# Optimization experiments

Hardware: AMD Instinct MI355X
Metric: run time of the kernel (lower is better)

Reference implementation:

```python
import jax, jax.numpy as jnp
import numpy as np

LN2 = 0.6931471805599453

def ssp(x):
    # 'shifted_sp' activation: softplus(x) - log(2)
    return jax.nn.softplus(x) - LN2

def _res_chain(x, W1, b1, W2, b2):
    # PhysNetResidual chain: x <- lin2(ssp(lin1(ssp(x)))) + x
    # W1/W2: [n_res, F, F], b1/b2: [n_res, F]
    for j in range(W1.shape[0]):
        h = ssp(x) @ W1[j] + b1[j]
        x = ssp(h) @ W2[j] + b2[j] + x
    return x

def _physnet_module(feat, radial_aev, idx12, p):
    (W_I, b_I, W_J, b_J, W_gate, gvec, W_int, b_int,
     ri_W1, ri_b1, ri_W2, ri_b2,
     ra_W1, ra_b1, ra_W2, ra_b2,
     ro_W1, ro_b1, ro_W2, ro_b2, W_out, b_out) = p
    N, F = feat.shape
    # self term (no species are dummy -> non_dummy indexing is identity)
    h_self = ssp(ssp(feat) @ W_I + b_I)                       # [N,F]
    # pair messages
    gate = radial_aev @ W_gate                                 # [P,F] (no bias)
    f12 = feat[idx12]                                          # [2,P,F] gather
    fm = ssp(ssp(f12) @ W_J + b_J)                             # [2,P,F]
    pair_msg = gate[None] * fm                                 # [2,P,F]
    proto = jnp.zeros_like(feat).at[idx12.reshape(-1)].add(
        pair_msg.reshape(-1, F))                               # scatter-add
    proto = proto + h_self
    msg = _res_chain(proto, ri_W1, ri_b1, ri_W2, ri_b2)
    feat2 = feat * gvec + ssp(msg) @ W_int + b_int
    feat2 = _res_chain(feat2, ra_W1, ra_b1, ra_W2, ra_b2)
    e = ssp(_res_chain(feat2, ro_W1, ro_b1, ro_W2, ro_b2)) @ W_out + b_out  # [N]
    return e, feat2

def setup_inputs() -> dict:
    key = jax.random.key(0)
    L, F, R = 5, 128, 64
    M, A = 128, 64
    N = M * A
    P = 400000
    ks = jax.random.split(key, 20)
    s = 0.05  # small weight scale keeps activations stable across 5 modules
    inp = {
        'species': jax.random.randint(ks[0], (M, A), 0, 4, dtype=jnp.int32),
        'features': jax.random.normal(ks[1], (N, F), jnp.float32),
        'radial_aev': jax.random.uniform(ks[2], (P, R), jnp.float32),
        'atom_index12': jax.random.randint(ks[3], (2, P), 0, N, dtype=jnp.int32),
        'W_I': jax.random.normal(ks[4], (L, F, F)) * s,
        'b_I': jnp.zeros((L, F)),
        'W_J': jax.random.normal(ks[5], (L, F, F)) * s,
        'b_J': jnp.zeros((L, F)),
        'W_gate': jax.random.normal(ks[6], (L, R, F)) * s,
        'gvec': jnp.ones((L, F)),
        'W_int': jax.random.normal(ks[7], (L, F, F)) * s,
        'b_int': jnp.zeros((L, F)),
        'ri_W1': jax.random.normal(ks[8], (L, 3, F, F)) * s,
        'ri_b1': jnp.zeros((L, 3, F)),
        'ri_W2': jax.random.normal(ks[9], (L, 3, F, F)) * s,
        'ri_b2': jnp.zeros((L, 3, F)),
        'ra_W1': jax.random.normal(ks[10], (L, 2, F, F)) * s,
        'ra_b1': jnp.zeros((L, 2, F)),
        'ra_W2': jax.random.normal(ks[11], (L, 2, F, F)) * s,
        'ra_b2': jnp.zeros((L, 2, F)),
        'ro_W1': jax.random.normal(ks[12], (L, 1, F, F)) * s,
        'ro_b1': jnp.zeros((L, 1, F)),
        'ro_W2': jax.random.normal(ks[13], (L, 1, F, F)) * s,
        'ro_b2': jnp.zeros((L, 1, F)),
        'W_out': jax.random.normal(ks[14], (L, F)) * s,
        'b_out': jnp.zeros((L,)),
    }
    return inp

def reference(species, features, radial_aev, atom_index12,
              W_I, b_I, W_J, b_J, W_gate, gvec, W_int, b_int,
              ri_W1, ri_b1, ri_W2, ri_b2,
              ra_W1, ra_b1, ra_W2, ra_b2,
              ro_W1, ro_b1, ro_W2, ro_b2, W_out, b_out):
    M, A = species.shape
    params = (W_I, b_I, W_J, b_J, W_gate, gvec, W_int, b_int,
              ri_W1, ri_b1, ri_W2, ri_b2,
              ra_W1, ra_b1, ra_W2, ra_b2,
              ro_W1, ro_b1, ro_W2, ro_b2, W_out, b_out)
    feat = features
    energies = jnp.zeros((M * A,), features.dtype)
    for l in range(W_I.shape[0]):  # fixed small module loop
        p = tuple(arr[l] for arr in params)
        e, feat = _physnet_module(feat, radial_aev, atom_index12, p)
        energies = energies + e
    return energies.reshape(M, A), feat
```

## Files before the change

### kernel.cpp

```cpp
#include <hip/hip_runtime.h>


#define LN2F 0.69314718055994530942f
#define NB 128

using short8  = __attribute__((ext_vector_type(8))) short;
using float4v = __attribute__((ext_vector_type(4))) float;

__device__ __forceinline__ float sspf(float x) {
  float ax = fabsf(x);
  return fmaxf(x, 0.0f) + __logf(1.0f + __expf(-ax)) - LN2F;
}

__device__ __forceinline__ unsigned short f2bf(float x) {
  return (unsigned short)((__float_as_uint(x) + 0x8000u) >> 16);
}

__device__ __forceinline__ unsigned short f2bf_ne(float x) {
  unsigned int u = __float_as_uint(x);
  u += 0x7fffu + ((u >> 16) & 1u);
  return (unsigned short)(u >> 16);
}

struct K1Args {
  const float* wsrc[80];
  int isgate[80];
  const float* bp[17];
  int bstride[17];
  const float* b_out;
  const int* idx;
  unsigned short* Wt;
  float* bias_pack;
  unsigned int* H;
  int n2p, C;
};

__global__ __launch_bounds__(256) void k1_prep(K1Args K) {
  __shared__ unsigned int h[8192];
  int b = blockIdx.x, tid = threadIdx.x;
  if (b < 80) {
    const float* s = K.wsrc[b];
    unsigned short* d = K.Wt + (size_t)b * 16384;
    if (!K.isgate[b]) {
      for (int it = 0; it < 8; ++it) {
        int id = tid + it * 256;
        int lane = id & 63, mm = (id >> 6) & 3, c8 = id >> 8;
        int l16 = lane & 15, quad = lane >> 4;
        int n = 16 * c8 + l16, k0 = 8 * (4 * mm + quad);
        unsigned short tmp[8];
#pragma unroll
        for (int cc = 0; cc < 8; ++cc) tmp[cc] = f2bf_ne(s[(k0 + cc) * 128 + n]);
        *(uint4*)(d + c8 * 2048 + mm * 512 + lane * 8) = *(uint4*)tmp;
      }
    } else {
      for (int it = 0; it < 4; ++it) {
        int id = tid + it * 256;
        int lane = id & 63, mm = (id >> 6) & 1, c8 = id >> 7;
        int l16 = lane & 15, quad = lane >> 4;
        int n = 16 * c8 + l16, k0 = 8 * (4 * mm + quad);
        unsigned short tmp[8];
#pragma unroll
        for (int cc = 0; cc < 8; ++cc) tmp[cc] = f2bf_ne(s[(k0 + cc) * 128 + n]);
        *(uint4*)(d + c8 * 1024 + mm * 512 + lane * 8) = *(uint4*)tmp;
      }
    }
  } else if (b < 85) {
    int l = b - 80;
    for (int i = tid; i < 17 * 128; i += 256) {
      int s = i >> 7;
      K.bias_pack[(size_t)l * 2304 + i] = K.bp[s][l * K.bstride[s] + (i & 127)];
    }
    if (tid == 0) K.bias_pack[(size_t)l * 2304 + 17 * 128] = K.b_out[l];
  } else {
    int blk = b - 85;
    for (int i = tid; i < 8192; i += 256) h[i] = 0;
    __syncthreads();
    int s = blk * K.C, e = min(s + K.C, K.n2p);
    for (int i = s + tid; i < e; i += 256) atomicAdd(&h[K.idx[i]], 1u);
    __syncthreads();
    for (int i = tid; i < 8192; i += 256) K.H[(size_t)blk * 8192 + i] = h[i];
  }
}

__global__ __launch_bounds__(256) void col_scan(unsigned int* __restrict__ H,
                                                unsigned int* __restrict__ tot) {
  int a = blockIdx.x * 256 + threadIdx.x;
  unsigned int run = 0;
  for (int b = 0; b < NB; ++b) {
    unsigned int v = H[(size_t)b * 8192 + a];
    H[(size_t)b * 8192 + a] = run;
    run += v;
  }
  tot[a] = run;
}

__global__ __launch_bounds__(256) void place_pass(const int* __restrict__ idx,
                                                  const unsigned int* __restrict__ H,
                                                  const unsigned int* __restrict__ tot,
                                                  unsigned int* __restrict__ off_out,
                                                  unsigned int* __restrict__ pairid,
                                                  int P, int C) {
  __shared__ unsigned int pos[8192];
  __shared__ unsigned int wt4[4];
  int b = blockIdx.x, tid = threadIdx.x;
  unsigned int local[32], s = 0;
#pragma unroll
  for (int i = 0; i < 32; ++i) { local[i] = tot[tid * 32 + i]; s += local[i]; }
  unsigned int v = s;
  int lane = tid & 63, wv = tid >> 6;
#pragma unroll
  for (int o = 1; o < 64; o <<= 1) {
    unsigned int u = __shfl_up(v, o, 64);
    if (lane >= o) v += u;
  }
  if (lane == 63) wt4[wv] = v;
  __syncthreads();
  unsigned int base = 0;
  for (int k = 0; k < wv; ++k) base += wt4[k];
  unsigned int excl = base + v - s;
#pragma unroll
  for (int i = 0; i < 32; ++i) {
    pos[tid * 32 + i] = excl;
    if (b == 0) off_out[tid * 32 + i] = excl;
    excl += local[i];
  }
  if (b == 0 && tid == 255) off_out[8192] = excl;
  __syncthreads();
  for (int i = tid; i < 8192; i += 256) pos[i] += H[(size_t)b * 8192 + i];
  __syncthreads();
  int n2p = 2 * P;
  int s2 = b * C, e2 = min(s2 + C, n2p);
  for (int i = s2 + tid; i < e2; i += 256) {
    int a = idx[i];
    unsigned int p = atomicAdd(&pos[a], 1u);
    pairid[p] = (i >= P) ? (unsigned int)(i - P) : (unsigned int)i;
  }
}

__global__ __launch_bounds__(256) void gather_kernel(const float* __restrict__ radial,
                                                     const unsigned int* __restrict__ off,
                                                     const unsigned int* __restrict__ pairid,
                                                     float* __restrict__ S) {
  __shared__ float4v red[3][16];
  int a = blockIdx.x;
  int lane = threadIdx.x & 63, w = threadIdx.x >> 6;
  int grp = lane >> 4, l16v = lane & 15;
  unsigned int b = off[a], e = off[a + 1];
  float4v acc = {0.f, 0.f, 0.f, 0.f};
  for (unsigned int base = b; base < e; base += 128) {
    unsigned int pp[8];
#pragma unroll
    for (int k = 0; k < 8; ++k) {
      unsigned int j = base + k * 16 + w * 4 + grp;
      pp[k] = pairid[j < e ? j : b];
    }
    float4v vv[8];
#pragma unroll
    for (int k = 0; k < 8; ++k)
      vv[k] = *(const float4v*)(radial + (size_t)pp[k] * 64 + l16v * 4);
#pragma unroll
    for (int k = 0; k < 8; ++k) {
      unsigned int j = base + k * 16 + w * 4 + grp;
      if (j < e) acc += vv[k];
    }
  }
#pragma unroll
  for (int o = 16; o < 64; o <<= 1) {
#pragma unroll
    for (int cc = 0; cc < 4; ++cc) acc[cc] += __shfl_xor(acc[cc], o, 64);
  }
  if (w > 0 && grp == 0) red[w - 1][l16v] = acc;
  __syncthreads();
  if (w == 0 && grp == 0) {
    acc += red[0][l16v];
    acc += red[1][l16v];
    acc += red[2][l16v];
    *(float4v*)(S + (size_t)a * 64 + l16v * 4) = acc;
  }
}

struct ChainArgs {
  const float* feat_in;
  const float* S;
  const unsigned short* wt;
  const float* bias_pack;
  float* feat_out;
  float* energy;
};

#define MFMA_ __builtin_amdgcn_mfma_f32_16x16x32_bf16
#define APOFF 2176

#define BAR() { __builtin_amdgcn_sched_barrier(0); \
  asm volatile("s_waitcnt lgkmcnt(0)" ::: "memory"); \
  __builtin_amdgcn_s_barrier(); \
  __builtin_amdgcn_sched_barrier(0); }

#define LDW(WP, sp) { \
  const unsigned short* wp_ = (sp) + woff; \
  W[WP][0] = *(const short8*)(wp_); \
  W[WP][1] = *(const short8*)(wp_ + 512); \
  W[WP][2] = *(const short8*)(wp_ + 1024); \
  W[WP][3] = *(const short8*)(wp_ + 1536); }

#define BINI(ACC, B) { (ACC)[0] = (B); (ACC)[1] = (B); (ACC)[2] = (B); (ACC)[3] = (B); }

#define G128R(AP, WP, ACC) { \
  short8 a0_ = *(const short8*)(aB + (AP)*APOFF); \
  short8 a1_ = *(const short8*)(aB + (AP)*APOFF + 32); \
  short8 a2_ = *(const short8*)(aB + (AP)*APOFF + 64); \
  short8 a3_ = *(const short8*)(aB + (AP)*APOFF + 96); \
  ACC = MFMA_(a0_, W[WP][0], ACC, 0, 0, 0); \
  ACC = MFMA_(a1_, W[WP][1], ACC, 0, 0, 0); \
  ACC = MFMA_(a2_, W[WP][2], ACC, 0, 0, 0); \
  ACC = MFMA_(a3_, W[WP][3], ACC, 0, 0, 0); }

#define WSSPM(AP, V) { \
  wB[(AP)*APOFF]       = f2bf(sspf((V)[0])); \
  wB[(AP)*APOFF + 136] = f2bf(sspf((V)[1])); \
  wB[(AP)*APOFF + 272] = f2bf(sspf((V)[2])); \
  wB[(AP)*APOFF + 408] = f2bf(sspf((V)[3])); }

#define MODBODY(L, S0) { \
  const float* bp = A.bias_pack + (L) * 2304; \
  const unsigned short* wtp = A.wt + (size_t)(L) * 16 * 16384; \
  float bW[15]; \
  _Pragma("unroll") \
  for (int q = 0; q < 15; ++q) bW[q] = bp[q * 128 + col0]; \
  float gvv = bp[15 * 128 + col0], wvv = bp[16 * 128 + col0]; \
   \
  { LDW((S0)^1, wtp + 2*16384); \
    gG = Z; \
    { short8 s0_ = *(const short8*)(aS); short8 s1_ = *(const short8*)(aS + 32); \
      gG = MFMA_(s0_, GT0, gG, 0, 0, 0); \
      gG = MFMA_(s1_, GT1, gG, 0, 0, 0); } \
    BINI(fm, bW[0]); G128R(0, (S0), fm); \
    for (int r = 0; r < 4; ++r) fm[r] = sspf(fm[r]); } \
   \
  { LDW((S0), wtp + 3*16384); \
    if ((L) < 4) { \
      GT0 = *(const short8*)(wtp + 16*16384 + goff); \
      GT1 = *(const short8*)(wtp + 16*16384 + goff + 512); \
    } \
    BINI(t4, bW[1]); G128R(0, (S0)^1, t4); \
    for (int r = 0; r < 4; ++r) xf[r] = fm[r] * gG[r] + sspf(t4[r]); } \
  WSSPM(1, xf); BAR(); \
   \
  { LDW((S0)^1, wtp + 4*16384); BINI(t4, bW[2]); G128R(1, (S0), t4); } \
  WSSPM(0, t4); BAR(); \
  { LDW((S0), wtp + 5*16384); BINI(t4, bW[3]); G128R(0, (S0)^1, t4); \
    for (int r = 0; r < 4; ++r) xf[r] += t4[r]; } \
  WSSPM(1, xf); BAR(); \
  { LDW((S0)^1, wtp + 6*16384); BINI(t4, bW[4]); G128R(1, (S0), t4); } \
  WSSPM(0, t4); BAR(); \
  { LDW((S0), wtp + 7*16384); BINI(t4, bW[5]); G128R(0, (S0)^1, t4); \
    for (int r = 0; r < 4; ++r) xf[r] += t4[r]; } \
  WSSPM(1, xf); BAR(); \
  { LDW((S0)^1, wtp + 8*16384); BINI(t4, bW[6]); G128R(1, (S0), t4); } \
  WSSPM(0, t4); BAR(); \
  { LDW((S0), wtp + 9*16384); BINI(t4, bW[7]); G128R(0, (S0)^1, t4); \
    for (int r = 0; r < 4; ++r) xf[r] += t4[r]; } \
  WSSPM(1, xf); BAR(); \
   \
  { LDW((S0)^1, wtp + 10*16384); BINI(t4, bW[8]); G128R(1, (S0), t4); \
    for (int r = 0; r < 4; ++r) xf[r] = ff[r] * gvv + t4[r]; } \
  WSSPM(0, xf); BAR(); \
   \
  { LDW((S0), wtp + 11*16384); BINI(t4, bW[9]); G128R(0, (S0)^1, t4); } \
  WSSPM(1, t4); BAR(); \
  { LDW((S0)^1, wtp + 12*16384); BINI(t4, bW[10]); G128R(1, (S0), t4); \
    for (int r = 0; r < 4; ++r) xf[r] += t4[r]; } \
  WSSPM(0, xf); BAR(); \
  { LDW((S0), wtp + 13*16384); BINI(t4, bW[11]); G128R(0, (S0)^1, t4); } \
  WSSPM(1, t4); BAR(); \
  { LDW((S0)^1, wtp + 14*16384); BINI(t4, bW[12]); G128R(1, (S0), t4); \
    for (int r = 0; r < 4; ++r) xf[r] += t4[r]; } \
  WSSPM(0, xf); BAR(); \
  ff = xf; \
  if ((L) == 4) { \
    for (int r = 0; r < 4; ++r) \
      A.feat_out[(size_t)(row0 + quad*4 + r) * 128 + col0] = xf[r]; \
  } \
   \
  { LDW((S0), wtp + 15*16384); BINI(t4, bW[13]); G128R(0, (S0)^1, t4); } \
  WSSPM(1, t4); BAR(); \
   \
  { if ((L) < 4) LDW((S0)^1, wtp + 17*16384); \
    BINI(t4, bW[14]); G128R(1, (S0), t4); \
    p0 += sspf(xf[0] + t4[0]) * wvv; \
    p1 += sspf(xf[1] + t4[1]) * wvv; \
    p2 += sspf(xf[2] + t4[2]) * wvv; \
    p3 += sspf(xf[3] + t4[3]) * wvv; } \
  bsum += bp[17*128]; \
  BAR(); }

__global__ __launch_bounds__(512)
__attribute__((amdgpu_waves_per_eu(4, 4)))
void chain_kernel(ChainArgs A) {
  __shared__ __align__(16) unsigned short sA[2][16 * 136];
  __shared__ __align__(16) unsigned short sS[16 * 72];
  __shared__ float sE[16];

  const int tid  = threadIdx.x;
  const int row0 = blockIdx.x * 16;
  const int lane = tid & 63;
  const int c    = tid >> 6;
  const int l16  = lane & 15;
  const int quad = lane >> 4;
  const int col0 = 16 * c + l16;

  const int woff = c * 2048 + lane * 8;
  const int goff = c * 1024 + lane * 8;

  const unsigned short* aB = &sA[0][0] + l16 * 136 + quad * 8;
  unsigned short*       wB = &sA[0][0] + (quad * 4) * 136 + col0;
  const unsigned short* aS = &sS[0] + l16 * 72 + quad * 8;

  short8 GT0, GT1;
  short8 W[2][4];
  GT0 = *(const short8*)(A.wt + goff);
  GT1 = *(const short8*)(A.wt + goff + 512);
  LDW(0, A.wt + 16384);

  for (int i = tid; i < 16 * 64; i += 512) {
    int r = i >> 6, k = i & 63;
    sS[r * 72 + k] = f2bf(A.S[(size_t)(row0 + r) * 64 + k]);
  }
  for (int i = tid; i < 16 * 128; i += 512) {
    int r = i >> 7, k = i & 127;
    sA[0][r * 136 + k] = f2bf(sspf(A.feat_in[(size_t)(row0 + r) * 128 + k]));
  }
  float4v ff;
#pragma unroll
  for (int r = 0; r < 4; ++r)
    ff[r] = A.feat_in[(size_t)(row0 + quad * 4 + r) * 128 + col0];
  if (tid < 16) sE[tid] = 0.0f;
  __syncthreads();

  const float4v Z = {0.f, 0.f, 0.f, 0.f};
  float4v gG, fm, xf, t4;
  float p0 = 0.f, p1 = 0.f, p2 = 0.f, p3 = 0.f, bsum = 0.f;

  MODBODY(0, 0)
  MODBODY(1, 1)
  MODBODY(2, 0)
  MODBODY(3, 1)
  MODBODY(4, 0)

#pragma unroll
  for (int o = 1; o < 16; o <<= 1) {
    p0 += __shfl_xor(p0, o, 64);
    p1 += __shfl_xor(p1, o, 64);
    p2 += __shfl_xor(p2, o, 64);
    p3 += __shfl_xor(p3, o, 64);
  }
  if (l16 == 0) {
    atomicAdd(&sE[quad * 4 + 0], p0);
    atomicAdd(&sE[quad * 4 + 1], p1);
    atomicAdd(&sE[quad * 4 + 2], p2);
    atomicAdd(&sE[quad * 4 + 3], p3);
  }
  BAR();
  if (tid < 16) A.energy[row0 + tid] = sE[tid] + bsum;
}

extern "C" void kernel_launch(void* const* d_in, const int* in_sizes, int n_in,
                              void* d_out, int out_size, void* d_ws, size_t ws_size,
                              hipStream_t stream) {
  const float* features = (const float*)d_in[1];
  const float* radial   = (const float*)d_in[2];
  const int*   idx12    = (const int*)  d_in[3];
  const float* W_I    = (const float*)d_in[4];
  const float* b_I    = (const float*)d_in[5];
  const float* W_J    = (const float*)d_in[6];
  const float* b_J    = (const float*)d_in[7];
  const float* W_gate = (const float*)d_in[8];
  const float* gvec   = (const float*)d_in[9];
  const float* W_int  = (const float*)d_in[10];
  const float* b_int  = (const float*)d_in[11];
  const float* ri_W1  = (const float*)d_in[12];
  const float* ri_b1  = (const float*)d_in[13];
  const float* ri_W2  = (const float*)d_in[14];
  const float* ri_b2  = (const float*)d_in[15];
  const float* ra_W1  = (const float*)d_in[16];
  const float* ra_b1  = (const float*)d_in[17];
  const float* ra_W2  = (const float*)d_in[18];
  const float* ra_b2  = (const float*)d_in[19];
  const float* ro_W1  = (const float*)d_in[20];
  const float* ro_b1  = (const float*)d_in[21];
  const float* ro_W2  = (const float*)d_in[22];
  const float* ro_b2  = (const float*)d_in[23];
  const float* W_out  = (const float*)d_in[24];
  const float* b_out  = (const float*)d_in[25];

  const int N = in_sizes[1] / 128;
  const int P = in_sizes[3] / 2;
  const int L = in_sizes[25];
  const int n2p = 2 * P;
  const int C = (n2p + NB - 1) / NB;

  float* S = (float*)d_ws;
  float* bias_pack = S + (size_t)N * 64;
  unsigned short* Wt = (unsigned short*)(bias_pack + 5 * 2304);
  unsigned int* H      = (unsigned int*)(Wt + (size_t)80 * 16384);
  unsigned int* tot    = H + (size_t)NB * 8192;
  unsigned int* off    = tot + N;
  unsigned int* pairid = off + N + 4;

  K1Args k1;
  for (int l = 0; l < L; ++l) {
    const float* fx[16] = {
      W_gate + l * 8192,
      W_J + l * 16384, W_I + l * 16384,
      ri_W1 + (l * 3 + 0) * 16384, ri_W2 + (l * 3 + 0) * 16384,
      ri_W1 + (l * 3 + 1) * 16384, ri_W2 + (l * 3 + 1) * 16384,
      ri_W1 + (l * 3 + 2) * 16384, ri_W2 + (l * 3 + 2) * 16384,
      W_int + l * 16384,
      ra_W1 + (l * 2 + 0) * 16384, ra_W2 + (l * 2 + 0) * 16384,
      ra_W1 + (l * 2 + 1) * 16384, ra_W2 + (l * 2 + 1) * 16384,
      ro_W1 + l * 16384, ro_W2 + l * 16384 };
    for (int t = 0; t < 16; ++t) { k1.wsrc[l * 16 + t] = fx[t]; k1.isgate[l * 16 + t] = (t == 0); }
  }
  const float* bp[17] = { b_J, b_I,
    ri_b1, ri_b2, ri_b1 + 128, ri_b2 + 128, ri_b1 + 256, ri_b2 + 256,
    b_int, ra_b1, ra_b2, ra_b1 + 128, ra_b2 + 128, ro_b1, ro_b2, gvec, W_out };
  int st[17] = {128,128, 384,384,384,384,384,384, 128, 256,256,256,256, 128,128,128,128};
  for (int q = 0; q < 17; ++q) { k1.bp[q] = bp[q]; k1.bstride[q] = st[q]; }
  k1.b_out = b_out;
  k1.idx = idx12; k1.Wt = Wt; k1.bias_pack = bias_pack; k1.H = H;
  k1.n2p = n2p; k1.C = C;
  k1_prep<<<80 + 5 + NB, 256, 0, stream>>>(k1);

  col_scan<<<32, 256, 0, stream>>>(H, tot);
  place_pass<<<NB, 256, 0, stream>>>(idx12, H, tot, off, pairid, P, C);
  gather_kernel<<<N, 256, 0, stream>>>(radial, off, pairid, S);

  ChainArgs ca;
  ca.feat_in   = features;
  ca.S         = S;
  ca.wt        = Wt;
  ca.bias_pack = bias_pack;
  ca.energy    = (float*)d_out;
  ca.feat_out  = (float*)d_out + N;
  chain_kernel<<<N / 16, 512, 0, stream>>>(ca);
}
```

Before: 320.8 us.

## Parallelize column scan, use exp2/log2 softplus and packed bf16 conversion

The column scan over the per-block histograms becomes a two-level scan: 256 blocks each handle 32 columns, with 8 row segments combined through shared memory, replacing 32 blocks that each walked all 128 rows serially. The shifted softplus now uses exp2/log2 with folded constants. The bf16 conversion in the activation write path uses the hardware packed instruction v_cvt_pk_bf16_f32, which rounds to nearest-even instead of the old round-half-up bit trick, so low bits can differ slightly. The scan reads H twice, trading extra memory traffic for much more parallelism.

```diff
diff --git a/kernel.cpp b/kernel.cpp
--- a/kernel.cpp
+++ b/kernel.cpp
@@ -2,14 +2,16 @@
 
 
 #define LN2F 0.69314718055994530942f
+#define L2EF 1.44269504088896340736f
 #define NB 128
 
 using short8  = __attribute__((ext_vector_type(8))) short;
 using float4v = __attribute__((ext_vector_type(4))) float;
 
 __device__ __forceinline__ float sspf(float x) {
-  float ax = fabsf(x);
-  return fmaxf(x, 0.0f) + __logf(1.0f + __expf(-ax)) - LN2F;
+  float t = exp2f(-L2EF * fabsf(x));
+  float l = log2f(1.0f + t);
+  return fmaxf(x, 0.0f) + fmaf(LN2F, l, -LN2F);
 }
 
 __device__ __forceinline__ unsigned short f2bf(float x) {
@@ -84,14 +86,33 @@
 
 __global__ __launch_bounds__(256) void col_scan(unsigned int* __restrict__ H,
                                                 unsigned int* __restrict__ tot) {
-  int a = blockIdx.x * 256 + threadIdx.x;
-  unsigned int run = 0;
-  for (int b = 0; b < NB; ++b) {
-    unsigned int v = H[(size_t)b * 8192 + a];
-    H[(size_t)b * 8192 + a] = run;
+  __shared__ unsigned int part[8][33];
+  int c = threadIdx.x & 31, r8 = threadIdx.x >> 5;
+  int col = blockIdx.x * 32 + c;
+  unsigned int psum = 0;
+#pragma unroll 4
+  for (int r = r8 * 16; r < r8 * 16 + 16; ++r)
+    psum += H[(size_t)r * 8192 + col];
+  part[r8][c] = psum;
+  __syncthreads();
+  if (threadIdx.x < 32) {
+    unsigned int run = 0;
+#pragma unroll
+    for (int s = 0; s < 8; ++s) {
+      unsigned int v = part[s][threadIdx.x];
+      part[s][threadIdx.x] = run;
+      run += v;
+    }
+    tot[blockIdx.x * 32 + threadIdx.x] = run;
+  }
+  __syncthreads();
+  unsigned int run = part[r8][c];
+#pragma unroll 4
+  for (int r = r8 * 16; r < r8 * 16 + 16; ++r) {
+    unsigned int v = H[(size_t)r * 8192 + col];
+    H[(size_t)r * 8192 + col] = run;
     run += v;
   }
-  tot[a] = run;
 }
 
 __global__ __launch_bounds__(256) void place_pass(const int* __restrict__ idx,
@@ -216,10 +237,15 @@
   ACC = MFMA_(a3_, W[WP][3], ACC, 0, 0, 0); }
 
 #define WSSPM(AP, V) { \
-  wB[(AP)*APOFF]       = f2bf(sspf((V)[0])); \
-  wB[(AP)*APOFF + 136] = f2bf(sspf((V)[1])); \
-  wB[(AP)*APOFF + 272] = f2bf(sspf((V)[2])); \
-  wB[(AP)*APOFF + 408] = f2bf(sspf((V)[3])); }
+  float s0_ = sspf((V)[0]), s1_ = sspf((V)[1]); \
+  float s2_ = sspf((V)[2]), s3_ = sspf((V)[3]); \
+  unsigned int p01_, p23_; \
+  asm("v_cvt_pk_bf16_f32 %0, %1, %2" : "=v"(p01_) : "v"(s0_), "v"(s1_)); \
+  asm("v_cvt_pk_bf16_f32 %0, %1, %2" : "=v"(p23_) : "v"(s2_), "v"(s3_)); \
+  wB[(AP)*APOFF]       = (unsigned short)p01_; \
+  wB[(AP)*APOFF + 136] = (unsigned short)(p01_ >> 16); \
+  wB[(AP)*APOFF + 272] = (unsigned short)p23_; \
+  wB[(AP)*APOFF + 408] = (unsigned short)(p23_ >> 16); }
 
 #define MODBODY(L, S0) { \
   const float* bp = A.bias_pack + (L) * 2304; \
@@ -431,7 +457,7 @@
   k1.n2p = n2p; k1.C = C;
   k1_prep<<<80 + 5 + NB, 256, 0, stream>>>(k1);
 
-  col_scan<<<32, 256, 0, stream>>>(H, tot);
+  col_scan<<<256, 256, 0, stream>>>(H, tot);
   place_pass<<<NB, 256, 0, stream>>>(idx12, H, tot, off, pairid, P, C);
   gather_kernel<<<N, 256, 0, stream>>>(radial, off, pairid, S);
 
```

Measured after the change: 318.8 us, median of 2. About the same (-0.6%).
